# Kernel tuning notes

Hardware: AMD Instinct MI355X
Metric: run time of the kernel (lower is better)

Reference implementation:

```python
import jax, jax.numpy as jnp
import numpy as np

S = 7
BB = 2          # boxes per cell
C = 20          # classes
L_COORD = 5.0
L_NOOBJ = 0.5
L_OBJ = 1.0
L_CLASS = 1.0
BATCH = 8192


def setup_inputs() -> dict:
    key = jax.random.key(0)
    k1, k2, k3, k4 = jax.random.split(key, 4)
    pred = jax.random.normal(k1, (BATCH, S, S, BB * 5 + C), dtype=jnp.float32)
    cls = jax.random.uniform(k2, (BATCH, S, S, C), dtype=jnp.float32)
    # obj conf must be exactly 1.0 where an object exists (obj_mask test is ==1)
    conf = (jax.random.uniform(k3, (BATCH, S, S, 1)) < 0.3).astype(jnp.float32)
    box = jax.random.uniform(k4, (BATCH, S, S, 4), dtype=jnp.float32)  # cx,cy,w,h in [0,1)
    target = jnp.concatenate([cls, conf, box], axis=-1)
    return {"pred": pred, "target": target}


def _iou(a, b):
    # a: (..., BB, 4) cx,cy,w,h ; b: (..., 1, 4)  -> iou (..., BB)
    ax1, ay1 = a[..., 0] - a[..., 2] / 2, a[..., 1] - a[..., 3] / 2
    ax2, ay2 = a[..., 0] + a[..., 2] / 2, a[..., 1] + a[..., 3] / 2
    bx1, by1 = b[..., 0] - b[..., 2] / 2, b[..., 1] - b[..., 3] / 2
    bx2, by2 = b[..., 0] + b[..., 2] / 2, b[..., 1] + b[..., 3] / 2
    iw = jnp.clip(jnp.minimum(ax2, bx2) - jnp.maximum(ax1, bx1), 0.0)
    ih = jnp.clip(jnp.minimum(ay2, by2) - jnp.maximum(ay1, by1), 0.0)
    inter = iw * ih
    union = jnp.abs(a[..., 2] * a[..., 3]) + jnp.abs(b[..., 2] * b[..., 3]) - inter
    return inter / (union + 1e-6)


def reference(pred, target):
    # pred: (N,S,S,B*5+C), target: (N,S,S,5+C)
    objf = (target[..., C] == 1.0).astype(pred.dtype)        # (N,S,S)
    noobjf = 1.0 - objf
    pred_boxes = pred[..., C:].reshape(-1, S, S, BB, 5)       # (N,S,S,B,5) [conf,cx,cy,w,h]
    tb = target[..., C:]                                      # (N,S,S,5)

    ious = _iou(pred_boxes[..., 1:], tb[..., None, 1:])       # (N,S,S,B)
    best = jnp.argmax(ious, axis=-1)                          # responsible box index
    iou_best = jnp.max(ious, axis=-1)                         # (N,S,S)
    pb = jnp.take_along_axis(pred_boxes, best[..., None, None], axis=3)[..., 0, :]  # (N,S,S,5)

    center = jnp.sum((tb[..., 1:3] - pb[..., 1:3]) ** 2, axis=-1)
    # pred wh: pow(2).sqrt().sqrt() == sqrt(|wh|)
    wh = jnp.sum((jnp.sqrt(tb[..., 3:]) - jnp.sqrt(jnp.abs(pb[..., 3:]))) ** 2, axis=-1)
    conf_sq = (tb[..., 0] - pb[..., 0]) ** 2
    cls_sq = jnp.sum((pred[..., :C] - target[..., :C]) ** 2, axis=-1)

    loss = jnp.sum(
        objf * (L_COORD * (center + wh) + L_OBJ * conf_sq + L_CLASS * cls_sq)
        + noobjf * L_NOOBJ * conf_sq
    )
    avg_iou = jnp.sum(iou_best * objf) / jnp.maximum(jnp.sum(objf), 1.0)
    return loss, avg_iou
```

## Files before the change

### kernel.cpp

```cpp
#include <hip/hip_runtime.h>
#include <stdint.h>

#define S 7
#define BB 2
#define CLS 20
#define NCELLS (8192 * S * S)
#define CPB 64
#define THREADS 64
#define NBLK (NCELLS / CPB)
#define PRED_F 30
#define TGT_F 25

#define ASYNC_CP16(gsrc, ldst)                                                  \
    __builtin_amdgcn_global_load_lds(                                           \
        (const __attribute__((address_space(1))) void*)(gsrc),                  \
        (__attribute__((address_space(3))) void*)(ldst), 16, 0, 0)

__device__ __forceinline__ float iou_fn(float ax, float ay, float aw, float ah,
                                        float bx, float by, float bw, float bh) {
    float ax1 = ax - aw * 0.5f, ay1 = ay - ah * 0.5f;
    float ax2 = ax + aw * 0.5f, ay2 = ay + ah * 0.5f;
    float bx1 = bx - bw * 0.5f, by1 = by - bh * 0.5f;
    float bx2 = bx + bw * 0.5f, by2 = by + bh * 0.5f;
    float iw = fmaxf(fminf(ax2, bx2) - fmaxf(ax1, bx1), 0.0f);
    float ih = fmaxf(fminf(ay2, by2) - fmaxf(ay1, by1), 0.0f);
    float inter = iw * ih;
    float uni = fabsf(aw * ah) + fabsf(bw * bh) - inter;
    return inter / (uni + 1e-6f);
}

__global__ __launch_bounds__(THREADS) void yolo_main(const float* __restrict__ pred,
                                                     const float* __restrict__ tgt,
                                                     float4* __restrict__ part) {
    __shared__ float lp[CPB * PRED_F];
    __shared__ float lt[CPB * TGT_F];

    const int b = blockIdx.x;
    const int t = threadIdx.x;

    const float* gp = pred + (size_t)b * (CPB * PRED_F) + t * 4;
    #pragma unroll
    for (int i = 0; i < 7; ++i) {
        ASYNC_CP16(gp + i * 256, lp + i * 256);
    }
    if (t < 32) {
        ASYNC_CP16(gp + 7 * 256, lp + 7 * 256);
    }
    const float* gt = tgt + (size_t)b * (CPB * TGT_F) + t * 4;
    #pragma unroll
    for (int i = 0; i < 6; ++i) {
        ASYNC_CP16(gt + i * 256, lt + i * 256);
    }
    if (t < 16) {
        ASYNC_CP16(gt + 6 * 256, lt + 6 * 256);
    }
    __syncthreads();

    const float* pp = lp + t * PRED_F;
    const float* tp = lt + t * TGT_F;

    float tconf = tp[CLS + 0];
    float tx = tp[CLS + 1], ty = tp[CLS + 2], tw = tp[CLS + 3], th = tp[CLS + 4];

    float iou0 = iou_fn(pp[CLS + 1], pp[CLS + 2], pp[CLS + 3], pp[CLS + 4], tx, ty, tw, th);
    float iou1 = iou_fn(pp[CLS + 6], pp[CLS + 7], pp[CLS + 8], pp[CLS + 9], tx, ty, tw, th);
    int sel = (iou1 > iou0) ? 1 : 0;
    float iou_best = fmaxf(iou0, iou1);

    const float* pb = pp + CLS + sel * 5;
    float dx = tx - pb[1], dy = ty - pb[2];
    float center = dx * dx + dy * dy;
    float dw = sqrtf(tw) - sqrtf(fabsf(pb[3]));
    float dh = sqrtf(th) - sqrtf(fabsf(pb[4]));
    float wh = dw * dw + dh * dh;
    float dc = tconf - pb[0];
    float conf_sq = dc * dc;

    float cls_sq = 0.0f;
    #pragma unroll
    for (int k = 0; k < CLS; ++k) {
        float d = pp[k] - tp[k];
        cls_sq += d * d;
    }

    float objf = (tconf == 1.0f) ? 1.0f : 0.0f;
    float loss = objf * (5.0f * (center + wh) + conf_sq + cls_sq)
               + (1.0f - objf) * 0.5f * conf_sq;
    float iou_o = objf * iou_best;

    #pragma unroll
    for (int off = 32; off > 0; off >>= 1) {
        loss  += __shfl_down(loss,  off, 64);
        iou_o += __shfl_down(iou_o, off, 64);
        objf  += __shfl_down(objf,  off, 64);
    }
    if (t == 0) {
        part[b] = make_float4(loss, iou_o, objf, 0.0f);
    }
}

__global__ __launch_bounds__(1024) void yolo_fin(const float4* __restrict__ part,
                                                 float* __restrict__ out) {
    __shared__ float red[3][1024 / 64];
    float l = 0.f, i = 0.f, o = 0.f;
    for (int k = threadIdx.x; k < NBLK; k += 1024) {
        float4 v = part[k];
        l += v.x;
        i += v.y;
        o += v.z;
    }
    #pragma unroll
    for (int off = 32; off > 0; off >>= 1) {
        l += __shfl_down(l, off, 64);
        i += __shfl_down(i, off, 64);
        o += __shfl_down(o, off, 64);
    }
    const int wave = threadIdx.x >> 6, lane = threadIdx.x & 63;
    if (lane == 0) {
        red[0][wave] = l;
        red[1][wave] = i;
        red[2][wave] = o;
    }
    __syncthreads();
    if (threadIdx.x == 0) {
        float L = 0.f, I = 0.f, O = 0.f;
        #pragma unroll
        for (int w = 0; w < 1024 / 64; ++w) {
            L += red[0][w];
            I += red[1][w];
            O += red[2][w];
        }
        out[0] = L;
        out[1] = I / fmaxf(O, 1.0f);
    }
}

extern "C" void kernel_launch(void* const* d_in, const int* in_sizes, int n_in,
                              void* d_out, int out_size, void* d_ws, size_t ws_size,
                              hipStream_t stream) {
    const float* pred = (const float*)d_in[0];
    const float* tgt  = (const float*)d_in[1];
    float* out = (float*)d_out;
    float4* part = (float4*)d_ws;

    yolo_main<<<NBLK, THREADS, 0, stream>>>(pred, tgt, part);
    yolo_fin<<<1, 1024, 0, stream>>>(part, out);
}
```

Measured before the change: 105.7 us.

## Process four chunks per block with double-buffered async LDS staging

Each block now handles four 64-cell chunks, strided across the grid, and accumulates their partial sums locally. The next chunk is staged into a second LDS buffer with global_load_lds while the current one is computed, using manual s_waitcnt counters in place of __syncthreads. This cuts the block count and the number of partials the final kernel reads, and is meant to hide load latency. The cost is twice the LDS per block and reliance on exact vmcnt accounting, since the block has a single wave and no barrier.

```diff
diff --git a/kernel.cpp b/kernel.cpp
--- a/kernel.cpp
+++ b/kernel.cpp
@@ -7,9 +7,10 @@
 #define NCELLS (8192 * S * S)
 #define CPB 64
 #define THREADS 64
-#define NBLK (NCELLS / CPB)
 #define PRED_F 30
 #define TGT_F 25
+#define NCHUNK 4
+#define NBLK_P (NCELLS / (CPB * NCHUNK))
 
 #define ASYNC_CP16(gsrc, ldst)                                                  \
     __builtin_amdgcn_global_load_lds(                                           \
@@ -32,70 +33,84 @@
 __global__ __launch_bounds__(THREADS) void yolo_main(const float* __restrict__ pred,
                                                      const float* __restrict__ tgt,
                                                      float4* __restrict__ part) {
-    __shared__ float lp[CPB * PRED_F];
-    __shared__ float lt[CPB * TGT_F];
+    __shared__ float lp[2][CPB * PRED_F];
+    __shared__ float lt[2][CPB * TGT_F];
 
     const int b = blockIdx.x;
     const int t = threadIdx.x;
 
-    const float* gp = pred + (size_t)b * (CPB * PRED_F) + t * 4;
+    auto stage = [&](int buf, int chunk) {
+        const float* gp = pred + (size_t)chunk * (CPB * PRED_F) + t * 4;
+        float* dp = &lp[buf][0];
+        #pragma unroll
+        for (int i = 0; i < 7; ++i) ASYNC_CP16(gp + i * 256, dp + i * 256);
+        if (t < 32) ASYNC_CP16(gp + 7 * 256, dp + 7 * 256);
+        const float* gt0 = tgt + (size_t)chunk * (CPB * TGT_F) + t * 4;
+        float* dt = &lt[buf][0];
+        #pragma unroll
+        for (int i = 0; i < 6; ++i) ASYNC_CP16(gt0 + i * 256, dt + i * 256);
+        if (t < 16) ASYNC_CP16(gt0 + 6 * 256, dt + 6 * 256);
+    };
+
+    float loss = 0.0f, iou_o = 0.0f, objs = 0.0f;
+
+    stage(0, b);
+
     #pragma unroll
-    for (int i = 0; i < 7; ++i) {
-        ASYNC_CP16(gp + i * 256, lp + i * 256);
+    for (int i = 0; i < NCHUNK; ++i) {
+        const int buf = i & 1;
+        if (i + 1 < NCHUNK) {
+            asm volatile("s_waitcnt lgkmcnt(0)" ::: "memory");
+            stage(buf ^ 1, b + (i + 1) * NBLK_P);
+            asm volatile("s_waitcnt vmcnt(15)" ::: "memory");
+        } else {
+            asm volatile("s_waitcnt vmcnt(0)" ::: "memory");
+        }
+
+        const float* pp = &lp[buf][t * PRED_F];
+        const float* tp = &lt[buf][t * TGT_F];
+
+        float tconf = tp[CLS + 0];
+        float tx = tp[CLS + 1], ty = tp[CLS + 2], tw = tp[CLS + 3], th = tp[CLS + 4];
+
+        float iou0 = iou_fn(pp[CLS + 1], pp[CLS + 2], pp[CLS + 3], pp[CLS + 4],
+                            tx, ty, tw, th);
+        float iou1 = iou_fn(pp[CLS + 6], pp[CLS + 7], pp[CLS + 8], pp[CLS + 9],
+                            tx, ty, tw, th);
+        int sel = (iou1 > iou0) ? 1 : 0;
+        float iou_best = fmaxf(iou0, iou1);
+
+        const float* pb = pp + CLS + sel * 5;
+        float dx = tx - pb[1], dy = ty - pb[2];
+        float center = dx * dx + dy * dy;
+        float dw = sqrtf(tw) - sqrtf(fabsf(pb[3]));
+        float dh = sqrtf(th) - sqrtf(fabsf(pb[4]));
+        float wh = dw * dw + dh * dh;
+        float dc = tconf - pb[0];
+        float conf_sq = dc * dc;
+
+        float cls_sq = 0.0f;
+        #pragma unroll
+        for (int k = 0; k < CLS; ++k) {
+            float d = pp[k] - tp[k];
+            cls_sq += d * d;
+        }
+
+        float objf = (tconf == 1.0f) ? 1.0f : 0.0f;
+        loss  += objf * (5.0f * (center + wh) + conf_sq + cls_sq)
+               + (1.0f - objf) * 0.5f * conf_sq;
+        iou_o += objf * iou_best;
+        objs  += objf;
     }
-    if (t < 32) {
-        ASYNC_CP16(gp + 7 * 256, lp + 7 * 256);
-    }
-    const float* gt = tgt + (size_t)b * (CPB * TGT_F) + t * 4;
-    #pragma unroll
-    for (int i = 0; i < 6; ++i) {
-        ASYNC_CP16(gt + i * 256, lt + i * 256);
-    }
-    if (t < 16) {
-        ASYNC_CP16(gt + 6 * 256, lt + 6 * 256);
-    }
-    __syncthreads();
-
-    const float* pp = lp + t * PRED_F;
-    const float* tp = lt + t * TGT_F;
-
-    float tconf = tp[CLS + 0];
-    float tx = tp[CLS + 1], ty = tp[CLS + 2], tw = tp[CLS + 3], th = tp[CLS + 4];
-
-    float iou0 = iou_fn(pp[CLS + 1], pp[CLS + 2], pp[CLS + 3], pp[CLS + 4], tx, ty, tw, th);
-    float iou1 = iou_fn(pp[CLS + 6], pp[CLS + 7], pp[CLS + 8], pp[CLS + 9], tx, ty, tw, th);
-    int sel = (iou1 > iou0) ? 1 : 0;
-    float iou_best = fmaxf(iou0, iou1);
-
-    const float* pb = pp + CLS + sel * 5;
-    float dx = tx - pb[1], dy = ty - pb[2];
-    float center = dx * dx + dy * dy;
-    float dw = sqrtf(tw) - sqrtf(fabsf(pb[3]));
-    float dh = sqrtf(th) - sqrtf(fabsf(pb[4]));
-    float wh = dw * dw + dh * dh;
-    float dc = tconf - pb[0];
-    float conf_sq = dc * dc;
-
-    float cls_sq = 0.0f;
-    #pragma unroll
-    for (int k = 0; k < CLS; ++k) {
-        float d = pp[k] - tp[k];
-        cls_sq += d * d;
-    }
-
-    float objf = (tconf == 1.0f) ? 1.0f : 0.0f;
-    float loss = objf * (5.0f * (center + wh) + conf_sq + cls_sq)
-               + (1.0f - objf) * 0.5f * conf_sq;
-    float iou_o = objf * iou_best;
 
     #pragma unroll
     for (int off = 32; off > 0; off >>= 1) {
         loss  += __shfl_down(loss,  off, 64);
         iou_o += __shfl_down(iou_o, off, 64);
-        objf  += __shfl_down(objf,  off, 64);
+        objs  += __shfl_down(objs,  off, 64);
     }
     if (t == 0) {
-        part[b] = make_float4(loss, iou_o, objf, 0.0f);
+        part[b] = make_float4(loss, iou_o, objs, 0.0f);
     }
 }
 
@@ -103,7 +118,7 @@
                                                  float* __restrict__ out) {
     __shared__ float red[3][1024 / 64];
     float l = 0.f, i = 0.f, o = 0.f;
-    for (int k = threadIdx.x; k < NBLK; k += 1024) {
+    for (int k = threadIdx.x; k < NBLK_P; k += 1024) {
         float4 v = part[k];
         l += v.x;
         i += v.y;
@@ -143,6 +158,6 @@
     float* out = (float*)d_out;
     float4* part = (float4*)d_ws;
 
-    yolo_main<<<NBLK, THREADS, 0, stream>>>(pred, tgt, part);
+    yolo_main<<<NBLK_P, THREADS, 0, stream>>>(pred, tgt, part);
     yolo_fin<<<1, 1024, 0, stream>>>(part, out);
 }
```

New measurement: 108.2 us. 1.02x slower.
